# Kernel tuning notes

Measured on AMD Instinct MI355X. Metric: run time of the kernel, lower is better.

The kernel has to match this reference:

```python
import jax, jax.numpy as jnp
import numpy as np

N = 100000
E = 3200000
F_IN = 128
H = 16
NUM_GRAPHS = 1000


def gcn_conv(x, W, b, src, dst, norm, n_nodes):
    # x: [N, Fin] -> h: [N, Fout]; gather along src, scale, scatter-add to dst
    h = x @ W
    msg = h[src] * norm[:, None]            # [E_tot, Fout]
    out = jax.ops.segment_sum(msg, dst, num_segments=n_nodes)
    return out + b


def setup_inputs() -> dict:
    key = jax.random.key(0)
    k0, k1, k2, k3, k4, k5 = jax.random.split(key, 6)
    x = jax.random.normal(k0, (N, F_IN), dtype=jnp.float32)
    edge_index = jax.random.randint(k1, (2, E), 0, N, dtype=jnp.int64)
    batch = jnp.sort(jax.random.randint(k2, (N,), 0, NUM_GRAPHS, dtype=jnp.int64))
    # Glorot-style init for GCN weights, zero bias (PyG default)
    W1 = jax.random.normal(k3, (F_IN, H), dtype=jnp.float32) / np.sqrt(F_IN)
    b1 = jnp.zeros((H,), dtype=jnp.float32)
    W2 = jax.random.normal(k4, (H, 1), dtype=jnp.float32) / np.sqrt(H)
    b2 = jnp.zeros((1,), dtype=jnp.float32)
    return {"x": x, "edge_index": edge_index, "batch": batch,
            "W1": W1, "b1": b1, "W2": W2, "b2": b2}


def reference(x, edge_index, batch, W1, b1, W2, b2):
    n_nodes = x.shape[0]
    # add self-loops (PyG GCNConv default)
    loop = jnp.arange(n_nodes, dtype=edge_index.dtype)
    src = jnp.concatenate([edge_index[0], loop])
    dst = jnp.concatenate([edge_index[1], loop])
    # symmetric normalization D^{-1/2} (A+I) D^{-1/2}
    deg = jax.ops.segment_sum(jnp.ones_like(dst, dtype=x.dtype), dst,
                              num_segments=n_nodes)
    dinv = jnp.where(deg > 0, jax.lax.rsqrt(deg), 0.0)
    norm = dinv[src] * dinv[dst]            # [E_tot]

    h = gcn_conv(x, W1, b1, src, dst, norm, n_nodes)   # [N, 16]
    h = jax.nn.relu(h)
    h = gcn_conv(h, W2, b2, src, dst, norm, n_nodes)   # [N, 1]
    # global_add_pool over graphs
    out = jax.ops.segment_sum(h, batch, num_segments=NUM_GRAPHS)  # [G, 1]
    return out
```

## Files before the change

### kernel.cpp

```cpp
#include <hip/hip_runtime.h>

#define NB_MAX   512
#define CHUNK    8192
#define CAPB     16384
#define SORT_CAP 12288

__device__ inline unsigned short f2bf(float f) {
    unsigned u = __float_as_uint(f);
    u += 0x7FFFu + ((u >> 16) & 1u);
    return (unsigned short)(u >> 16);
}

__global__ void k_zero(float* __restrict__ out, int g, int* __restrict__ bcnt) {
    int t = blockIdx.x * blockDim.x + threadIdx.x;
    if (t < g) out[t] = 0.f;
    if (t < NB_MAX) bcnt[t] = 0;
}

__global__ __launch_bounds__(512) void k_scatter(const int* __restrict__ src,
                                                 const int* __restrict__ dst,
                                                 int* __restrict__ bcnt,
                                                 int* __restrict__ packed,
                                                 int E) {
    __shared__ int lh[NB_MAX];
    __shared__ int ldelta[NB_MAX];
    __shared__ int wsum[8];
    __shared__ int sorted[CHUNK];
    __shared__ unsigned short sbkt[CHUNK];
    int t = threadIdx.x;
    int e0 = blockIdx.x * CHUNK;
    int e1 = min(e0 + CHUNK, E);
    int cnt = e1 - e0;
    lh[t] = 0;
    __syncthreads();
    int pv[16], bv[16];
#pragma unroll
    for (int j = 0; j < 16; j++) {
        int e = e0 + t + j * 512;
        bool ok = e < e1;
        int d = ok ? dst[e] : 0;
        int sv = ok ? src[e] : 0;
        int b = d >> 8;
        pv[j] = sv | ((d & 255) << 24);
        bv[j] = ok ? b : -1;
        if (ok) atomicAdd(&lh[b], 1);
    }
    __syncthreads();
    int v = lh[t];
    int lane = t & 63, wid = t >> 6;
    int s = v;
#pragma unroll
    for (int o = 1; o < 64; o <<= 1) {
        int u = __shfl_up(s, o, 64);
        if (lane >= o) s += u;
    }
    if (lane == 63) wsum[wid] = s;
    __syncthreads();
    int base = 0;
#pragma unroll
    for (int w = 0; w < 8; w++) base += (w < wid) ? wsum[w] : 0;
    int ex = s + base - v;
    int gbase = v ? atomicAdd(&bcnt[t], v) : 0;
    lh[t] = ex;
    ldelta[t] = t * CAPB + gbase - ex;
    __syncthreads();
#pragma unroll
    for (int j = 0; j < 16; j++) {
        int b = bv[j];
        if (b >= 0) {
            int r = atomicAdd(&lh[b], 1);
            sorted[r] = pv[j];
            sbkt[r] = (unsigned short)b;
        }
    }
    __syncthreads();
    for (int i = t; i < cnt; i += 512)
        packed[i + ldelta[sbkt[i]]] = sorted[i];
}

__global__ __launch_bounds__(512) void k_sortgemm(const int* __restrict__ packed,
                                                  const int* __restrict__ bcnt,
                                                  const float* __restrict__ x,
                                                  const float* __restrict__ W1,
                                                  int* __restrict__ sidx2,
                                                  int* __restrict__ noffs,
                                                  int* __restrict__ ndeg,
                                                  float* __restrict__ dinv,
                                                  unsigned short* __restrict__ hs,
                                                  int n) {
    __shared__ int hist[256];
    __shared__ int curs[256];
    __shared__ int wsum[4];
    __shared__ float sdinv[256];
    __shared__ float sW[128 * 16];
    __shared__ __align__(16) char smem[SORT_CAP * 4];
    int* sorted = (int*)smem;
    float* sXT = (float*)smem;

    int t = threadIdx.x, b = blockIdx.x;
    int seg0 = b * CAPB, cnt = bcnt[b];
    int node0 = b << 8;

    float4 xreg[4];
#pragma unroll
    for (int pass = 0; pass < 4; pass++) {
        int row = pass * 64 + (t >> 3);
        int node = node0 + row;
        xreg[pass] = *(const float4*)(x + (size_t)min(node, n - 1) * 128 + (t & 7) * 4);
    }

    for (int q = t; q < 2048; q += 512) sW[q] = W1[q];
    if (t < 256) hist[t] = 0;
    __syncthreads();
    int pv[16];
#pragma unroll
    for (int j = 0; j < 16; j++) {
        int e = t + j * 512;
        bool ok = e < cnt;
        int p = ok ? packed[seg0 + e] : 0;
        pv[j] = p;
        if (ok) atomicAdd(&hist[(unsigned)p >> 24], 1);
    }
    for (int e = CHUNK + t; e < cnt; e += 512)
        atomicAdd(&hist[(unsigned)packed[seg0 + e] >> 24], 1);
    __syncthreads();
    int v = 0, s = 0;
    if (t < 256) { v = hist[t]; s = v; }
    int lane = t & 63, wid = t >> 6;
#pragma unroll
    for (int o = 1; o < 64; o <<= 1) {
        int u = __shfl_up(s, o, 64);
        if (lane >= o) s += u;
    }
    if (t < 256 && lane == 63) wsum[wid] = s;
    __syncthreads();
    int ex = 0;
    if (t < 256) {
        int base = 0;
#pragma unroll
        for (int w = 0; w < 4; w++) base += (w < wid) ? wsum[w] : 0;
        ex = s + base - v;
        float di = rsqrtf((float)v + 1.0f);
        sdinv[t] = di;
        int node = node0 + t;
        if (node < n) {
            noffs[node] = seg0 + ex;
            ndeg[node] = v;
            dinv[node] = di;
        }
    }
    if (cnt <= SORT_CAP) {
        if (t < 256) curs[t] = ex;
        __syncthreads();
#pragma unroll
        for (int j = 0; j < 16; j++) {
            int e = t + j * 512;
            if (e < cnt) {
                int p = pv[j];
                int r = atomicAdd(&curs[(unsigned)p >> 24], 1);
                sorted[r] = p & 0xFFFFFF;
            }
        }
        for (int e = CHUNK + t; e < cnt; e += 512) {
            int p = packed[seg0 + e];
            int r = atomicAdd(&curs[(unsigned)p >> 24], 1);
            sorted[r] = p & 0xFFFFFF;
        }
        __syncthreads();
        for (int i = t; i < cnt; i += 512)
            sidx2[seg0 + i] = sorted[i];
    } else {
        if (t < 256) curs[t] = seg0 + ex;
        __syncthreads();
        for (int e = t; e < cnt; e += 512) {
            int p = packed[seg0 + e];
            int dl = (int)((unsigned)p >> 24);
            int r = atomicAdd(&curs[dl], 1);
            sidx2[r] = p & 0xFFFFFF;
        }
    }

    int ng = t >> 2, cg = t & 3;
    float acc[2][4];
#pragma unroll
    for (int i = 0; i < 2; i++)
#pragma unroll
        for (int j = 0; j < 4; j++) acc[i][j] = 0.f;
    for (int kc = 0; kc < 4; kc++) {
        __syncthreads();
#pragma unroll
        for (int pass = 0; pass < 4; pass++) {
            int row = pass * 64 + (t >> 3);
            int k0 = (t & 7) * 4;
            sXT[(k0 + 0) * 260 + row] = xreg[pass].x;
            sXT[(k0 + 1) * 260 + row] = xreg[pass].y;
            sXT[(k0 + 2) * 260 + row] = xreg[pass].z;
            sXT[(k0 + 3) * 260 + row] = xreg[pass].w;
        }
        if (kc < 3) {
#pragma unroll
            for (int pass = 0; pass < 4; pass++) {
                int row = pass * 64 + (t >> 3);
                int node = node0 + row;
                xreg[pass] = *(const float4*)(x + (size_t)min(node, n - 1) * 128
                                              + (kc + 1) * 32 + (t & 7) * 4);
            }
        }
        __syncthreads();
        const float* wbase = sW + kc * 32 * 16 + cg * 4;
#pragma unroll 8
        for (int k = 0; k < 32; k++) {
            float2 xv = *(const float2*)&sXT[k * 260 + ng * 2];
            float4 wv = *(const float4*)&wbase[k * 16];
            acc[0][0] += xv.x * wv.x; acc[0][1] += xv.x * wv.y;
            acc[0][2] += xv.x * wv.z; acc[0][3] += xv.x * wv.w;
            acc[1][0] += xv.y * wv.x; acc[1][1] += xv.y * wv.y;
            acc[1][2] += xv.y * wv.z; acc[1][3] += xv.y * wv.w;
        }
    }
#pragma unroll
    for (int i = 0; i < 2; i++) {
        int local = ng * 2 + i;
        int node = node0 + local;
        if (node < n) {
            float di = sdinv[local];
            ushort4 o;
            o.x = f2bf(acc[i][0] * di);
            o.y = f2bf(acc[i][1] * di);
            o.z = f2bf(acc[i][2] * di);
            o.w = f2bf(acc[i][3] * di);
            *(ushort4*)&hs[(size_t)node * 16 + cg * 4] = o;
        }
    }
}

#define UNPACK_ADD2(u)                                       \
    acc[0] += __uint_as_float((u).x << 16);                  \
    acc[1] += __uint_as_float((u).x & 0xFFFF0000u);          \
    acc[2] += __uint_as_float((u).y << 16);                  \
    acc[3] += __uint_as_float((u).y & 0xFFFF0000u);

__global__ __launch_bounds__(256) void k_agg1(const uint2* __restrict__ hs2,
                                              const int* __restrict__ noffs,
                                              const int* __restrict__ ndeg,
                                              const int* __restrict__ sidx2,
                                              const float* __restrict__ dinv,
                                              const float* __restrict__ b1,
                                              const float* __restrict__ W2,
                                              float* __restrict__ hw, int n) {
    int tid = blockIdx.x * 256 + threadIdx.x;
    int node = tid >> 2, q = tid & 3;
    if (node >= n) return;
    float acc[4];
    uint2 u0 = hs2[(size_t)node * 4 + q];
    acc[0] = __uint_as_float(u0.x << 16);
    acc[1] = __uint_as_float(u0.x & 0xFFFF0000u);
    acc[2] = __uint_as_float(u0.y << 16);
    acc[3] = __uint_as_float(u0.y & 0xFFFF0000u);
    int e0 = noffs[node], e1 = e0 + ndeg[node];
    int e = e0;
    for (; e + 7 < e1; e += 8) {
        int s0 = sidx2[e],     s1 = sidx2[e + 1];
        int s2 = sidx2[e + 2], s3 = sidx2[e + 3];
        int s4 = sidx2[e + 4], s5 = sidx2[e + 5];
        int s6 = sidx2[e + 6], s7 = sidx2[e + 7];
        uint2 a0 = hs2[(size_t)s0 * 4 + q];
        uint2 a1 = hs2[(size_t)s1 * 4 + q];
        uint2 a2 = hs2[(size_t)s2 * 4 + q];
        uint2 a3 = hs2[(size_t)s3 * 4 + q];
        uint2 a4 = hs2[(size_t)s4 * 4 + q];
        uint2 a5 = hs2[(size_t)s5 * 4 + q];
        uint2 a6 = hs2[(size_t)s6 * 4 + q];
        uint2 a7 = hs2[(size_t)s7 * 4 + q];
        UNPACK_ADD2(a0) UNPACK_ADD2(a1) UNPACK_ADD2(a2) UNPACK_ADD2(a3)
        UNPACK_ADD2(a4) UNPACK_ADD2(a5) UNPACK_ADD2(a6) UNPACK_ADD2(a7)
    }
    for (; e < e1; e++) {
        uint2 a = hs2[(size_t)sidx2[e] * 4 + q];
        UNPACK_ADD2(a)
    }
    float di = dinv[node];
    int base = q * 4;
    float r = 0.f;
#pragma unroll
    for (int j = 0; j < 4; j++)
        r += fmaxf(di * acc[j] + b1[base + j], 0.f) * W2[base + j];
    r += __shfl_down(r, 2, 4);
    r += __shfl_down(r, 1, 4);
    if (q == 0) hw[node] = r * di;
}

__global__ __launch_bounds__(256) void k_agg2(const float* __restrict__ hw,
                                              const int* __restrict__ noffs,
                                              const int* __restrict__ ndeg,
                                              const int* __restrict__ sidx2,
                                              const float* __restrict__ dinv,
                                              const float* __restrict__ b2,
                                              const int* __restrict__ batch,
                                              float* __restrict__ out, int n) {
    __shared__ float v[128];
    __shared__ int g[128];
    int t = threadIdx.x;
    int tid = blockIdx.x * 256 + t;
    int i = tid >> 1, q = tid & 1;
    int li = t >> 1;
    float acc = 0.f;
    int gid = -1;
    if (i < n) {
        if (q == 0) acc = hw[i];
        int e0 = noffs[i], e1 = e0 + ndeg[i];
        int e = e0 + q;
        for (; e + 6 < e1; e += 8)
            acc += hw[sidx2[e]] + hw[sidx2[e + 2]] + hw[sidx2[e + 4]] + hw[sidx2[e + 6]];
        for (; e < e1; e += 2) acc += hw[sidx2[e]];
    }
    acc += __shfl_down(acc, 1, 2);
    if (q == 0) {
        if (i < n) {
            v[li] = dinv[i] * acc + b2[0];
            g[li] = batch[i];
        } else {
            v[li] = 0.f;
            g[li] = -1;
        }
    }
    __syncthreads();
    if (q == 0) {
        int gid2 = g[li];
        if (gid2 >= 0 && (li == 0 || g[li - 1] != gid2)) {
            float sum = v[li];
            for (int w = li + 1; w < 128 && g[w] == gid2; w++) sum += v[w];
            atomicAdd(&out[gid2], sum);
        }
    }
}

extern "C" void kernel_launch(void* const* d_in, const int* in_sizes, int n_in,
                              void* d_out, int out_size, void* d_ws, size_t ws_size,
                              hipStream_t stream) {
    int n = in_sizes[0] / 128;
    int E = in_sizes[1] / 2;
    const float* x     = (const float*)d_in[0];
    const int*   ei    = (const int*)d_in[1];
    const int*   src   = ei;
    const int*   dst   = ei + E;
    const int*   batch = (const int*)d_in[2];
    const float* W1    = (const float*)d_in[3];
    const float* b1    = (const float*)d_in[4];
    const float* W2    = (const float*)d_in[5];
    const float* b2    = (const float*)d_in[6];
    float* out = (float*)d_out;

    int nb = (n + 255) >> 8;

    char* p = (char*)d_ws;
    auto carve = [&](size_t bytes) {
        void* r = (void*)p;
        p += (bytes + 63) & ~(size_t)63;
        return r;
    };
    int*            bcnt   = (int*)carve(NB_MAX * 4);
    int*            packed = (int*)carve((size_t)nb * CAPB * 4);
    int*            sidx2  = (int*)carve((size_t)nb * CAPB * 4);
    int*            noffs  = (int*)carve((size_t)n * 4);
    int*            ndeg   = (int*)carve((size_t)n * 4);
    float*          dinv   = (float*)carve((size_t)n * 4);
    unsigned short* hs     = (unsigned short*)carve((size_t)n * 16 * 2);
    float*          hw     = (float*)carve((size_t)n * 4);

    k_zero<<<(out_size + 1023) / 1024, 1024, 0, stream>>>(out, out_size, bcnt);
    k_scatter<<<(E + CHUNK - 1) / CHUNK, 512, 0, stream>>>(src, dst, bcnt, packed, E);
    k_sortgemm<<<nb, 512, 0, stream>>>(packed, bcnt, x, W1, sidx2, noffs, ndeg,
                                       dinv, hs, n);
    k_agg1<<<((size_t)n * 4 + 255) / 256, 256, 0, stream>>>((const uint2*)hs, noffs, ndeg,
                                                            sidx2, dinv, b1, W2, hw, n);
    k_agg2<<<((size_t)n * 2 + 255) / 256, 256, 0, stream>>>(hw, noffs, ndeg, sidx2,
                                                            dinv, b2, batch, out, n);
}
```

Baseline: 114.6 us.

## Split per-bucket sort+GEMM across two blocks and halve scatter chunk size

k_sortgemm now launches two blocks per 256-node destination bucket. Each block scans the whole bucket's packed edges but only histograms, sorts and writes the edges for its own 128-node half, placing them at a base offset inside the bucket. It then computes the x·W1 product for its 128 nodes with one node per thread group. k_scatter processes 4096-edge chunks instead of 8192, which doubles its block count. Both changes aim to expose more blocks and reduce per-block work and shared memory on a GPU with many CUs. The cost is that the packed bucket is read twice and more global bucket-count atomics are issued.

```diff
diff --git a/kernel.cpp b/kernel.cpp
--- a/kernel.cpp
+++ b/kernel.cpp
@@ -1,9 +1,9 @@
 #include <hip/hip_runtime.h>
 
 #define NB_MAX   512
-#define CHUNK    8192
+#define CHUNK    4096
 #define CAPB     16384
-#define SORT_CAP 12288
+#define SORT_CAP 6144
 
 __device__ inline unsigned short f2bf(float f) {
     unsigned u = __float_as_uint(f);
@@ -33,9 +33,9 @@
     int cnt = e1 - e0;
     lh[t] = 0;
     __syncthreads();
-    int pv[16], bv[16];
-#pragma unroll
-    for (int j = 0; j < 16; j++) {
+    int pv[8], bv[8];
+#pragma unroll
+    for (int j = 0; j < 8; j++) {
         int e = e0 + t + j * 512;
         bool ok = e < e1;
         int d = ok ? dst[e] : 0;
@@ -65,7 +65,7 @@
     ldelta[t] = t * CAPB + gbase - ex;
     __syncthreads();
 #pragma unroll
-    for (int j = 0; j < 16; j++) {
+    for (int j = 0; j < 8; j++) {
         int b = bv[j];
         if (b >= 0) {
             int r = atomicAdd(&lh[b], 1);
@@ -88,149 +88,153 @@
                                                   float* __restrict__ dinv,
                                                   unsigned short* __restrict__ hs,
                                                   int n) {
-    __shared__ int hist[256];
-    __shared__ int curs[256];
-    __shared__ int wsum[4];
-    __shared__ float sdinv[256];
+    __shared__ int hist[128];
+    __shared__ int curs[128];
+    __shared__ int wsum2[2];
+    __shared__ int sh_ownbase, sh_owntot;
+    __shared__ float sdinv[128];
     __shared__ float sW[128 * 16];
     __shared__ __align__(16) char smem[SORT_CAP * 4];
     int* sorted = (int*)smem;
     float* sXT = (float*)smem;
 
-    int t = threadIdx.x, b = blockIdx.x;
+    int t = threadIdx.x, blk = blockIdx.x;
+    int b = blk >> 1, half = blk & 1;
     int seg0 = b * CAPB, cnt = bcnt[b];
-    int node0 = b << 8;
-
-    float4 xreg[4];
-#pragma unroll
-    for (int pass = 0; pass < 4; pass++) {
+    int node0h = blk << 7;
+
+    float4 xreg[2];
+#pragma unroll
+    for (int pass = 0; pass < 2; pass++) {
         int row = pass * 64 + (t >> 3);
-        int node = node0 + row;
-        xreg[pass] = *(const float4*)(x + (size_t)min(node, n - 1) * 128 + (t & 7) * 4);
-    }
-
+        xreg[pass] = *(const float4*)(x + (size_t)min(node0h + row, n - 1) * 128 + (t & 7) * 4);
+    }
     for (int q = t; q < 2048; q += 512) sW[q] = W1[q];
-    if (t < 256) hist[t] = 0;
+    if (t < 128) hist[t] = 0;
     __syncthreads();
     int pv[16];
 #pragma unroll
     for (int j = 0; j < 16; j++) {
         int e = t + j * 512;
-        bool ok = e < cnt;
-        int p = ok ? packed[seg0 + e] : 0;
+        int p = (e < cnt) ? packed[seg0 + e] : 0;
         pv[j] = p;
-        if (ok) atomicAdd(&hist[(unsigned)p >> 24], 1);
-    }
-    for (int e = CHUNK + t; e < cnt; e += 512)
-        atomicAdd(&hist[(unsigned)packed[seg0 + e] >> 24], 1);
+        if (e < cnt) {
+            int dl = (int)((unsigned)p >> 24);
+            if ((dl >> 7) == half) atomicAdd(&hist[dl & 127], 1);
+        }
+    }
+    for (int e = 8192 + t; e < cnt; e += 512) {
+        int p = packed[seg0 + e];
+        int dl = (int)((unsigned)p >> 24);
+        if ((dl >> 7) == half) atomicAdd(&hist[dl & 127], 1);
+    }
     __syncthreads();
     int v = 0, s = 0;
-    if (t < 256) { v = hist[t]; s = v; }
     int lane = t & 63, wid = t >> 6;
+    if (t < 128) { v = hist[t]; s = v; }
 #pragma unroll
     for (int o = 1; o < 64; o <<= 1) {
         int u = __shfl_up(s, o, 64);
         if (lane >= o) s += u;
     }
-    if (t < 256 && lane == 63) wsum[wid] = s;
-    __syncthreads();
-    int ex = 0;
-    if (t < 256) {
-        int base = 0;
-#pragma unroll
-        for (int w = 0; w < 4; w++) base += (w < wid) ? wsum[w] : 0;
-        ex = s + base - v;
+    if (t < 128 && lane == 63) wsum2[wid] = s;
+    __syncthreads();
+    if (t == 0) {
+        int tot = wsum2[0] + wsum2[1];
+        sh_owntot = tot;
+        sh_ownbase = half ? (cnt - tot) : 0;
+    }
+    __syncthreads();
+    int ownbase = sh_ownbase, owntot = sh_owntot;
+    if (t < 128) {
+        int base = (wid == 1) ? wsum2[0] : 0;
+        int ex = s + base - v;
+        curs[t] = ex;
         float di = rsqrtf((float)v + 1.0f);
         sdinv[t] = di;
-        int node = node0 + t;
+        int node = node0h + t;
         if (node < n) {
-            noffs[node] = seg0 + ex;
+            noffs[node] = seg0 + ownbase + ex;
             ndeg[node] = v;
             dinv[node] = di;
         }
     }
-    if (cnt <= SORT_CAP) {
-        if (t < 256) curs[t] = ex;
-        __syncthreads();
+    __syncthreads();
+    if (owntot <= SORT_CAP) {
 #pragma unroll
         for (int j = 0; j < 16; j++) {
             int e = t + j * 512;
             if (e < cnt) {
                 int p = pv[j];
-                int r = atomicAdd(&curs[(unsigned)p >> 24], 1);
+                int dl = (int)((unsigned)p >> 24);
+                if ((dl >> 7) == half) {
+                    int r = atomicAdd(&curs[dl & 127], 1);
+                    sorted[r] = p & 0xFFFFFF;
+                }
+            }
+        }
+        for (int e = 8192 + t; e < cnt; e += 512) {
+            int p = packed[seg0 + e];
+            int dl = (int)((unsigned)p >> 24);
+            if ((dl >> 7) == half) {
+                int r = atomicAdd(&curs[dl & 127], 1);
                 sorted[r] = p & 0xFFFFFF;
             }
         }
-        for (int e = CHUNK + t; e < cnt; e += 512) {
-            int p = packed[seg0 + e];
-            int r = atomicAdd(&curs[(unsigned)p >> 24], 1);
-            sorted[r] = p & 0xFFFFFF;
-        }
         __syncthreads();
-        for (int i = t; i < cnt; i += 512)
-            sidx2[seg0 + i] = sorted[i];
+        for (int i = t; i < owntot; i += 512)
+            sidx2[seg0 + ownbase + i] = sorted[i];
     } else {
-        if (t < 256) curs[t] = seg0 + ex;
-        __syncthreads();
         for (int e = t; e < cnt; e += 512) {
             int p = packed[seg0 + e];
             int dl = (int)((unsigned)p >> 24);
-            int r = atomicAdd(&curs[dl], 1);
-            sidx2[r] = p & 0xFFFFFF;
-        }
-    }
-
-    int ng = t >> 2, cg = t & 3;
-    float acc[2][4];
-#pragma unroll
-    for (int i = 0; i < 2; i++)
-#pragma unroll
-        for (int j = 0; j < 4; j++) acc[i][j] = 0.f;
+            if ((dl >> 7) == half) {
+                int r = atomicAdd(&curs[dl & 127], 1);
+                sidx2[seg0 + ownbase + r] = p & 0xFFFFFF;
+            }
+        }
+    }
+
+    int nd = t >> 2, cg = t & 3;
+    float acc[4] = {0.f, 0.f, 0.f, 0.f};
     for (int kc = 0; kc < 4; kc++) {
         __syncthreads();
 #pragma unroll
-        for (int pass = 0; pass < 4; pass++) {
+        for (int pass = 0; pass < 2; pass++) {
             int row = pass * 64 + (t >> 3);
             int k0 = (t & 7) * 4;
-            sXT[(k0 + 0) * 260 + row] = xreg[pass].x;
-            sXT[(k0 + 1) * 260 + row] = xreg[pass].y;
-            sXT[(k0 + 2) * 260 + row] = xreg[pass].z;
-            sXT[(k0 + 3) * 260 + row] = xreg[pass].w;
+            sXT[(k0 + 0) * 132 + row] = xreg[pass].x;
+            sXT[(k0 + 1) * 132 + row] = xreg[pass].y;
+            sXT[(k0 + 2) * 132 + row] = xreg[pass].z;
+            sXT[(k0 + 3) * 132 + row] = xreg[pass].w;
         }
         if (kc < 3) {
 #pragma unroll
-            for (int pass = 0; pass < 4; pass++) {
+            for (int pass = 0; pass < 2; pass++) {
                 int row = pass * 64 + (t >> 3);
-                int node = node0 + row;
-                xreg[pass] = *(const float4*)(x + (size_t)min(node, n - 1) * 128
+                xreg[pass] = *(const float4*)(x + (size_t)min(node0h + row, n - 1) * 128
                                               + (kc + 1) * 32 + (t & 7) * 4);
             }
         }
         __syncthreads();
-        const float* wbase = sW + kc * 32 * 16 + cg * 4;
+        const float* wb = sW + kc * 512 + cg * 4;
 #pragma unroll 8
         for (int k = 0; k < 32; k++) {
-            float2 xv = *(const float2*)&sXT[k * 260 + ng * 2];
-            float4 wv = *(const float4*)&wbase[k * 16];
-            acc[0][0] += xv.x * wv.x; acc[0][1] += xv.x * wv.y;
-            acc[0][2] += xv.x * wv.z; acc[0][3] += xv.x * wv.w;
-            acc[1][0] += xv.y * wv.x; acc[1][1] += xv.y * wv.y;
-            acc[1][2] += xv.y * wv.z; acc[1][3] += xv.y * wv.w;
-        }
-    }
-#pragma unroll
-    for (int i = 0; i < 2; i++) {
-        int local = ng * 2 + i;
-        int node = node0 + local;
-        if (node < n) {
-            float di = sdinv[local];
-            ushort4 o;
-            o.x = f2bf(acc[i][0] * di);
-            o.y = f2bf(acc[i][1] * di);
-            o.z = f2bf(acc[i][2] * di);
-            o.w = f2bf(acc[i][3] * di);
-            *(ushort4*)&hs[(size_t)node * 16 + cg * 4] = o;
-        }
+            float xs = sXT[k * 132 + nd];
+            float4 wv = *(const float4*)&wb[k * 16];
+            acc[0] += xs * wv.x; acc[1] += xs * wv.y;
+            acc[2] += xs * wv.z; acc[3] += xs * wv.w;
+        }
+    }
+    int node = node0h + nd;
+    if (node < n) {
+        float di = sdinv[nd];
+        ushort4 o;
+        o.x = f2bf(acc[0] * di);
+        o.y = f2bf(acc[1] * di);
+        o.z = f2bf(acc[2] * di);
+        o.w = f2bf(acc[3] * di);
+        *(ushort4*)&hs[(size_t)node * 16 + cg * 4] = o;
     }
 }
 
@@ -370,8 +374,8 @@
 
     k_zero<<<(out_size + 1023) / 1024, 1024, 0, stream>>>(out, out_size, bcnt);
     k_scatter<<<(E + CHUNK - 1) / CHUNK, 512, 0, stream>>>(src, dst, bcnt, packed, E);
-    k_sortgemm<<<nb, 512, 0, stream>>>(packed, bcnt, x, W1, sidx2, noffs, ndeg,
-                                       dinv, hs, n);
+    k_sortgemm<<<2 * nb, 512, 0, stream>>>(packed, bcnt, x, W1, sidx2, noffs, ndeg,
+                                           dinv, hs, n);
     k_agg1<<<((size_t)n * 4 + 255) / 256, 256, 0, stream>>>((const uint2*)hs, noffs, ndeg,
                                                             sidx2, dinv, b1, W2, hw, n);
     k_agg2<<<((size_t)n * 2 + 255) / 256, 256, 0, stream>>>(hw, noffs, ndeg, sidx2,
```

Result: slower. 122.0 us (+6.5%).
